# Optimization experiments

Measured on AMD Instinct MI355X. Metric: run time of the kernel, lower is better.

The kernel has to match this reference:

```python
import jax, jax.numpy as jnp
import numpy as np

N = 50000
E = 1600000
F_IN = 128
F_OUT = 64
NEG_SLOPE = 0.2


def setup_inputs() -> dict:
    key = jax.random.key(0)
    k1, k2, k3, k4, k5, k6 = jax.random.split(key, 6)
    x = jax.random.normal(k1, (N, F_IN), dtype=jnp.float32)
    edge_index = jax.random.randint(k2, (2, E), 0, N, dtype=jnp.int64)
    # GATConv params (heads=1): glorot-ish scale
    W = jax.random.normal(k3, (F_IN, F_OUT), dtype=jnp.float32) * (1.0 / np.sqrt(F_IN))
    att_src = jax.random.normal(k4, (F_OUT,), dtype=jnp.float32) * (1.0 / np.sqrt(F_OUT))
    att_dst = jax.random.normal(k5, (F_OUT,), dtype=jnp.float32) * (1.0 / np.sqrt(F_OUT))
    bias = jnp.zeros((F_OUT,), dtype=jnp.float32)
    return {"x": x, "edge_index": edge_index, "W": W, "att_src": att_src, "att_dst": att_dst, "bias": bias}


def _gat_forward(x, edge_index, W, att_src, att_dst, bias):
    n = x.shape[0]
    # add self loops (PyG GATConv default)
    loops = jnp.arange(n, dtype=edge_index.dtype)
    src = jnp.concatenate([edge_index[0], loops])  # [E+N]
    dst = jnp.concatenate([edge_index[1], loops])  # [E+N]

    h = x @ W                                      # [N, F_OUT]
    a_src = h @ att_src                            # [N]
    a_dst = h @ att_dst                            # [N]

    e = a_src[src] + a_dst[dst]                    # [E+N]
    e = jnp.where(e > 0, e, NEG_SLOPE * e)         # LeakyReLU(0.2)

    # softmax over edges grouped by destination node
    e_max = jax.ops.segment_max(e, dst, num_segments=n)     # [N]
    e_exp = jnp.exp(e - e_max[dst])                          # [E+N]
    e_sum = jax.ops.segment_sum(e_exp, dst, num_segments=n)  # [N]
    alpha = e_exp / e_sum[dst]                               # [E+N]

    msg = h[src] * alpha[:, None]                            # [E+N, F_OUT]
    out = jax.ops.segment_sum(msg, dst, num_segments=n)      # [N, F_OUT]
    out = out + bias
    return jax.nn.relu(out)


def reference(x, edge_index, W, att_src, att_dst, bias):
    return _gat_forward(x, edge_index, W, att_src, att_dst, bias)
```

## Files before the change

### kernel.cpp

```cpp
#include <hip/hip_runtime.h>

#define NN 50000
#define NE 1600000
#define FIN 128
#define FOUT 64
#define SLOPE 0.2f

#define NB   1563
#define NPB  32
#define CAPB 1536
#define FBLK 261
#define CHC4 1536
#define GBLK 782
#define LW   136

typedef unsigned int u32;
typedef short short8 __attribute__((ext_vector_type(8)));
typedef float f32x4 __attribute__((ext_vector_type(4)));

__device__ __forceinline__ unsigned short f2bf(float f) {
    u32 u = __float_as_uint(f);
    u += 0x7FFFu + ((u >> 16) & 1u);
    return (unsigned short)(u >> 16);
}
__device__ __forceinline__ float bf2f(unsigned short s) {
    return __uint_as_float(((u32)s) << 16);
}

union FusedLds {
    unsigned short Wt[64 * LW];
    struct { int lc[NB]; int lb[NB]; } f;
};

__global__ __launch_bounds__(256) void fused_k(
        const float* __restrict__ x, const float* __restrict__ W,
        const float* __restrict__ att_s, const float* __restrict__ att_d,
        const int* __restrict__ ei, int* __restrict__ bcur,
        u32* __restrict__ staging, unsigned short* __restrict__ h,
        float* __restrict__ a_src, float* __restrict__ a_dst) {
    __shared__ FusedLds L;
    const int tid = threadIdx.x;

    if (blockIdx.x < FBLK) {
        int* lc = L.f.lc; int* lb = L.f.lb;
        for (int j = tid; j < NB; j += 256) lc[j] = 0;
        __syncthreads();
        const int4* sd4 = (const int4*)(ei + NE);
        const int4* ss4 = (const int4*)ei;
        const int lo = blockIdx.x * CHC4, hi = min(NE / 4, lo + CHC4);
        for (int i = lo + tid; i < hi; i += 256) {
            int4 d = sd4[i];
            atomicAdd(&lc[d.x >> 5], 1);
            atomicAdd(&lc[d.y >> 5], 1);
            atomicAdd(&lc[d.z >> 5], 1);
            atomicAdd(&lc[d.w >> 5], 1);
        }
        __syncthreads();
        for (int j = tid; j < NB; j += 256) {
            int c = lc[j];
            lb[j] = c ? atomicAdd(&bcur[j], c) : 0;
        }
        __syncthreads();
        for (int j = tid; j < NB; j += 256) lc[j] = 0;
        __syncthreads();
        for (int i = lo + tid; i < hi; i += 256) {
            int4 d = sd4[i];
            int4 s = ss4[i];
            int b, pos;
            b = d.x >> 5; pos = lb[b] + atomicAdd(&lc[b], 1);
            if (pos < CAPB) staging[b * CAPB + pos] = (u32)s.x | ((u32)(d.x & 31) << 16);
            b = d.y >> 5; pos = lb[b] + atomicAdd(&lc[b], 1);
            if (pos < CAPB) staging[b * CAPB + pos] = (u32)s.y | ((u32)(d.y & 31) << 16);
            b = d.z >> 5; pos = lb[b] + atomicAdd(&lc[b], 1);
            if (pos < CAPB) staging[b * CAPB + pos] = (u32)s.z | ((u32)(d.z & 31) << 16);
            b = d.w >> 5; pos = lb[b] + atomicAdd(&lc[b], 1);
            if (pos < CAPB) staging[b * CAPB + pos] = (u32)s.w | ((u32)(d.w & 31) << 16);
        }
    } else {
        unsigned short* Wt = L.Wt;
        const int node0 = (blockIdx.x - FBLK) * 64;
        for (int i = tid; i < 128 * 16; i += 256) {
            int k = i >> 4, f = (i & 15) * 4;
            float4 w4 = ((const float4*)W)[i];
            Wt[(f + 0) * LW + k] = f2bf(w4.x);
            Wt[(f + 1) * LW + k] = f2bf(w4.y);
            Wt[(f + 2) * LW + k] = f2bf(w4.z);
            Wt[(f + 3) * LW + k] = f2bf(w4.w);
        }

        const int wv = tid >> 6, lane = tid & 63;
        const int q = lane >> 4, mr = lane & 15;
        const int row = node0 + wv * 16 + mr;
        const bool valid = row < NN;
        const float4* x4 = (const float4*)x;

        short8 afr[4];
        #pragma unroll
        for (int ks = 0; ks < 4; ++ks) {
            float4 f0 = make_float4(0.f, 0.f, 0.f, 0.f), f1 = f0;
            if (valid) {
                f0 = x4[(size_t)row * 32 + ks * 8 + q * 2];
                f1 = x4[(size_t)row * 32 + ks * 8 + q * 2 + 1];
            }
            short8 a;
            a[0] = (short)f2bf(f0.x); a[1] = (short)f2bf(f0.y);
            a[2] = (short)f2bf(f0.z); a[3] = (short)f2bf(f0.w);
            a[4] = (short)f2bf(f1.x); a[5] = (short)f2bf(f1.y);
            a[6] = (short)f2bf(f1.z); a[7] = (short)f2bf(f1.w);
            afr[ks] = a;
        }
        __syncthreads();

        f32x4 acc[4] = {{0,0,0,0},{0,0,0,0},{0,0,0,0},{0,0,0,0}};
        #pragma unroll
        for (int ks = 0; ks < 4; ++ks) {
            #pragma unroll
            for (int nt = 0; nt < 4; ++nt) {
                short8 b = *(const short8*)(Wt + (nt * 16 + mr) * LW + ks * 32 + q * 8);
                acc[nt] = __builtin_amdgcn_mfma_f32_16x16x32_bf16(afr[ks], b, acc[nt], 0, 0, 0);
            }
        }
        float atts[4], attd[4];
        #pragma unroll
        for (int nt = 0; nt < 4; ++nt) {
            atts[nt] = att_s[nt * 16 + mr];
            attd[nt] = att_d[nt * 16 + mr];
        }
        #pragma unroll
        for (int r = 0; r < 4; ++r) {
            int node = node0 + wv * 16 + q * 4 + r;
            float ps = 0.f, pd = 0.f;
            #pragma unroll
            for (int nt = 0; nt < 4; ++nt) {
                float v = acc[nt][r];
                if (node < NN) h[(size_t)node * 64 + nt * 16 + mr] = f2bf(v);
                ps += v * atts[nt];
                pd += v * attd[nt];
            }
            #pragma unroll
            for (int off = 8; off > 0; off >>= 1) {
                ps += __shfl_xor(ps, off);
                pd += __shfl_xor(pd, off);
            }
            if (mr == 0 && node < NN) { a_src[node] = ps; a_dst[node] = pd; }
        }
    }
}

__global__ __launch_bounds__(256) void agg_k(
        const u32* __restrict__ staging, const int* __restrict__ bcur,
        const float* __restrict__ a_src, const float* __restrict__ a_dst,
        const ushort4* __restrict__ h4, const float* __restrict__ bias,
        float* __restrict__ out) {
    const int bkt = blockIdx.x;
    const int node0 = bkt << 5;
    const int nNodes = min(NPB, NN - node0);
    const int bsize = min(bcur[bkt], CAPB);
    const u32* stg = staging + bkt * CAPB;
    const int tid = threadIdx.x, wv = tid >> 6, lane = tid & 63;

    __shared__ u32 pk[CAPB];
    __shared__ unsigned short ssrc[CAPB];
    __shared__ int lcnt[NPB];
    __shared__ int lbase[NPB + 1];
    __shared__ int lcur[NPB];
    float* evals = (float*)pk;

    for (int j = tid; j < bsize; j += 256) pk[j] = stg[j];
    if (tid < NPB) lcnt[tid] = 0;
    __syncthreads();
    for (int j = tid; j < bsize; j += 256)
        atomicAdd(&lcnt[pk[j] >> 16], 1);
    __syncthreads();
    if (tid < 64) {
        int v = (tid < NPB) ? lcnt[tid] : 0;
        #pragma unroll
        for (int off = 1; off < NPB; off <<= 1) {
            int u = __shfl_up(v, off);
            if (tid >= off) v += u;
        }
        if (tid < NPB) lbase[tid + 1] = v;
        if (tid == 0) lbase[0] = 0;
    }
    if (tid >= 64 && tid < 64 + NPB) lcur[tid - 64] = 0;
    __syncthreads();
    for (int j = tid; j < bsize; j += 256) {
        u32 w = pk[j];
        int ld = w >> 16;
        int pos = lbase[ld] + atomicAdd(&lcur[ld], 1);
        ssrc[pos] = (unsigned short)(w & 0xFFFFu);
    }
    __syncthreads();

    const int q = lane >> 4, ql = lane & 15;
    const float4 b4 = ((const float4*)bias)[ql];
    #pragma unroll
    for (int rnd = 0; rnd < 2; ++rnd) {
        const int ln = rnd * 16 + wv * 4 + q;
        if (ln >= nNodes) continue;
        const int n = node0 + ln;
        const int st = lbase[ln], deg = lbase[ln + 1] - st;
        const float ad = a_dst[n];
        float es = a_src[n] + ad; es = es > 0.f ? es : SLOPE * es;
        const float ps = __expf(es);
        float sum = 0.f;
        for (int j = ql; j < deg; j += 16) {
            int s = ssrc[st + j];
            float e = a_src[s] + ad; e = e > 0.f ? e : SLOPE * e;
            float pe = __expf(e);
            evals[st + j] = pe;
            sum += pe;
        }
        sum += __shfl_xor(sum, 8); sum += __shfl_xor(sum, 4);
        sum += __shfl_xor(sum, 2); sum += __shfl_xor(sum, 1);
        const float inv = 1.f / (sum + ps);

        ushort4 hs = h4[(size_t)n * 16 + ql];
        float a0 = ps * bf2f(hs.x), a1 = ps * bf2f(hs.y);
        float a2 = ps * bf2f(hs.z), a3 = ps * bf2f(hs.w);
        int j = 0;
        for (; j + 4 <= deg; j += 4) {
            int s0 = ssrc[st + j], s1 = ssrc[st + j + 1];
            int s2 = ssrc[st + j + 2], s3 = ssrc[st + j + 3];
            float e0 = evals[st + j], e1 = evals[st + j + 1];
            float e2 = evals[st + j + 2], e3 = evals[st + j + 3];
            ushort4 v0 = h4[(size_t)s0 * 16 + ql];
            ushort4 v1 = h4[(size_t)s1 * 16 + ql];
            ushort4 v2 = h4[(size_t)s2 * 16 + ql];
            ushort4 v3 = h4[(size_t)s3 * 16 + ql];
            a0 += e0 * bf2f(v0.x); a1 += e0 * bf2f(v0.y);
            a2 += e0 * bf2f(v0.z); a3 += e0 * bf2f(v0.w);
            a0 += e1 * bf2f(v1.x); a1 += e1 * bf2f(v1.y);
            a2 += e1 * bf2f(v1.z); a3 += e1 * bf2f(v1.w);
            a0 += e2 * bf2f(v2.x); a1 += e2 * bf2f(v2.y);
            a2 += e2 * bf2f(v2.z); a3 += e2 * bf2f(v2.w);
            a0 += e3 * bf2f(v3.x); a1 += e3 * bf2f(v3.y);
            a2 += e3 * bf2f(v3.z); a3 += e3 * bf2f(v3.w);
        }
        for (; j < deg; ++j) {
            int s = ssrc[st + j];
            float ev = evals[st + j];
            ushort4 hv = h4[(size_t)s * 16 + ql];
            a0 += ev * bf2f(hv.x); a1 += ev * bf2f(hv.y);
            a2 += ev * bf2f(hv.z); a3 += ev * bf2f(hv.w);
        }
        float4 o;
        o.x = a0 * inv + b4.x; o.x = o.x > 0.f ? o.x : 0.f;
        o.y = a1 * inv + b4.y; o.y = o.y > 0.f ? o.y : 0.f;
        o.z = a2 * inv + b4.z; o.z = o.z > 0.f ? o.z : 0.f;
        o.w = a3 * inv + b4.w; o.w = o.w > 0.f ? o.w : 0.f;
        ((float4*)out)[(size_t)n * 16 + ql] = o;
    }
}

extern "C" void kernel_launch(void* const* d_in, const int* in_sizes, int n_in,
                              void* d_out, int out_size, void* d_ws, size_t ws_size,
                              hipStream_t stream) {
    const float* x     = (const float*)d_in[0];
    const int*   ei    = (const int*)d_in[1];
    const float* W     = (const float*)d_in[2];
    const float* att_s = (const float*)d_in[3];
    const float* att_d = (const float*)d_in[4];
    const float* bias  = (const float*)d_in[5];
    float* out = (float*)d_out;

    unsigned short* h = (unsigned short*)d_ws;
    float* a_src  = (float*)(h + (size_t)NN * 64);
    float* a_dst  = a_src + NN;
    int*   bcur   = (int*)(a_dst + NN);
    u32*   staging = (u32*)(bcur + 2048);

    hipMemsetAsync(bcur, 0, NB * sizeof(int), stream);

    fused_k<<<FBLK + GBLK, 256, 0, stream>>>(x, W, att_s, att_d, ei, bcur,
                                             staging, h, a_src, a_dst);
    agg_k<<<NB, 256, 0, stream>>>(staging, bcur, a_src, a_dst,
                                  (const ushort4*)h, bias, out);
}
```

Before: 145.6 us.

## Replace single-pass bucket scatter with two-level coarse/fine radix partition of edges

Edge bucketing by destination now runs in two passes. A coarse pass scatters edges into 63 bins of 800 nodes each, with small per-wave LDS histograms, and a new fine_k kernel splits each bin into 32-node buckets for the aggregation kernel. The aim is to cut the global atomic traffic and scattered writes of the old scheme, which kept 1563 per-block counters and did one global atomic per bucket per block. The cost is an extra kernel launch and an extra read/write pass over the staged edges. Bucket capacity limits remain, so overflowing buckets would still silently drop edges.

```diff
diff --git a/kernel.cpp b/kernel.cpp
--- a/kernel.cpp
+++ b/kernel.cpp
@@ -6,12 +6,16 @@
 #define FOUT 64
 #define SLOPE 0.2f
 
-#define NB   1563
+#define NBC  63
+#define NPC  800
+#define CAPC 27500
+#define NBF  1575
 #define NPB  32
 #define CAPB 1536
 #define FBLK 261
 #define CHC4 1536
 #define GBLK 782
+#define K2PB 8
 #define LW   136
 
 typedef unsigned int u32;
@@ -29,52 +33,52 @@
 
 union FusedLds {
     unsigned short Wt[64 * LW];
-    struct { int lc[NB]; int lb[NB]; } f;
+    struct { int cnt[4][64]; int gb[64]; int cur[64]; } f;
 };
 
 __global__ __launch_bounds__(256) void fused_k(
         const float* __restrict__ x, const float* __restrict__ W,
         const float* __restrict__ att_s, const float* __restrict__ att_d,
-        const int* __restrict__ ei, int* __restrict__ bcur,
-        u32* __restrict__ staging, unsigned short* __restrict__ h,
+        const int* __restrict__ ei, int* __restrict__ ccur,
+        u32* __restrict__ cstage, unsigned short* __restrict__ h,
         float* __restrict__ a_src, float* __restrict__ a_dst) {
     __shared__ FusedLds L;
     const int tid = threadIdx.x;
 
     if (blockIdx.x < FBLK) {
-        int* lc = L.f.lc; int* lb = L.f.lb;
-        for (int j = tid; j < NB; j += 256) lc[j] = 0;
+        const int wv = tid >> 6;
+        ((int*)L.f.cnt)[tid] = 0;
         __syncthreads();
         const int4* sd4 = (const int4*)(ei + NE);
         const int4* ss4 = (const int4*)ei;
         const int lo = blockIdx.x * CHC4, hi = min(NE / 4, lo + CHC4);
         for (int i = lo + tid; i < hi; i += 256) {
             int4 d = sd4[i];
-            atomicAdd(&lc[d.x >> 5], 1);
-            atomicAdd(&lc[d.y >> 5], 1);
-            atomicAdd(&lc[d.z >> 5], 1);
-            atomicAdd(&lc[d.w >> 5], 1);
+            atomicAdd(&L.f.cnt[wv][d.x / NPC], 1);
+            atomicAdd(&L.f.cnt[wv][d.y / NPC], 1);
+            atomicAdd(&L.f.cnt[wv][d.z / NPC], 1);
+            atomicAdd(&L.f.cnt[wv][d.w / NPC], 1);
         }
         __syncthreads();
-        for (int j = tid; j < NB; j += 256) {
-            int c = lc[j];
-            lb[j] = c ? atomicAdd(&bcur[j], c) : 0;
-        }
-        __syncthreads();
-        for (int j = tid; j < NB; j += 256) lc[j] = 0;
+        if (tid < NBC) {
+            int tot = L.f.cnt[0][tid] + L.f.cnt[1][tid]
+                    + L.f.cnt[2][tid] + L.f.cnt[3][tid];
+            L.f.gb[tid] = tot ? atomicAdd(&ccur[tid], tot) : 0;
+            L.f.cur[tid] = 0;
+        }
         __syncthreads();
         for (int i = lo + tid; i < hi; i += 256) {
             int4 d = sd4[i];
             int4 s = ss4[i];
             int b, pos;
-            b = d.x >> 5; pos = lb[b] + atomicAdd(&lc[b], 1);
-            if (pos < CAPB) staging[b * CAPB + pos] = (u32)s.x | ((u32)(d.x & 31) << 16);
-            b = d.y >> 5; pos = lb[b] + atomicAdd(&lc[b], 1);
-            if (pos < CAPB) staging[b * CAPB + pos] = (u32)s.y | ((u32)(d.y & 31) << 16);
-            b = d.z >> 5; pos = lb[b] + atomicAdd(&lc[b], 1);
-            if (pos < CAPB) staging[b * CAPB + pos] = (u32)s.z | ((u32)(d.z & 31) << 16);
-            b = d.w >> 5; pos = lb[b] + atomicAdd(&lc[b], 1);
-            if (pos < CAPB) staging[b * CAPB + pos] = (u32)s.w | ((u32)(d.w & 31) << 16);
+            b = d.x / NPC; pos = L.f.gb[b] + atomicAdd(&L.f.cur[b], 1);
+            if (pos < CAPC) cstage[b * CAPC + pos] = (u32)s.x | ((u32)(d.x - b * NPC) << 16);
+            b = d.y / NPC; pos = L.f.gb[b] + atomicAdd(&L.f.cur[b], 1);
+            if (pos < CAPC) cstage[b * CAPC + pos] = (u32)s.y | ((u32)(d.y - b * NPC) << 16);
+            b = d.z / NPC; pos = L.f.gb[b] + atomicAdd(&L.f.cur[b], 1);
+            if (pos < CAPC) cstage[b * CAPC + pos] = (u32)s.z | ((u32)(d.z - b * NPC) << 16);
+            b = d.w / NPC; pos = L.f.gb[b] + atomicAdd(&L.f.cur[b], 1);
+            if (pos < CAPC) cstage[b * CAPC + pos] = (u32)s.w | ((u32)(d.w - b * NPC) << 16);
         }
     } else {
         unsigned short* Wt = L.Wt;
@@ -87,7 +91,6 @@
             Wt[(f + 2) * LW + k] = f2bf(w4.z);
             Wt[(f + 3) * LW + k] = f2bf(w4.w);
         }
-
         const int wv = tid >> 6, lane = tid & 63;
         const int q = lane >> 4, mr = lane & 15;
         const int row = node0 + wv * 16 + mr;
@@ -147,6 +150,41 @@
     }
 }
 
+__global__ __launch_bounds__(256) void fine_k(
+        const u32* __restrict__ cstage, const int* __restrict__ ccur,
+        int* __restrict__ fcur, u32* __restrict__ fstage) {
+    const int bin = blockIdx.x / K2PB, sub = blockIdx.x % K2PB;
+    const int size = min(ccur[bin], CAPC);
+    const int qs = (size + K2PB - 1) / K2PB;
+    const int lo = sub * qs, hi = min(size, lo + qs);
+    const u32* src = cstage + (size_t)bin * CAPC;
+    const int tid = threadIdx.x, wv = tid >> 6;
+
+    __shared__ int cnt[4][32];
+    __shared__ int gb[32];
+    __shared__ int cur[32];
+    ((int*)cnt)[tid & 127] = 0;
+    __syncthreads();
+    for (int i = lo + tid; i < hi; i += 256)
+        atomicAdd(&cnt[wv][(src[i] >> 16) >> 5], 1);
+    __syncthreads();
+    if (tid < 25) {
+        int tot = cnt[0][tid] + cnt[1][tid] + cnt[2][tid] + cnt[3][tid];
+        gb[tid] = tot ? atomicAdd(&fcur[bin * 25 + tid], tot) : 0;
+        cur[tid] = 0;
+    }
+    __syncthreads();
+    for (int i = lo + tid; i < hi; i += 256) {
+        u32 w = src[i];
+        int dl = w >> 16;
+        int f = dl >> 5;
+        int pos = gb[f] + atomicAdd(&cur[f], 1);
+        if (pos < CAPB)
+            fstage[(size_t)(bin * 25 + f) * CAPB + pos] =
+                (w & 0xFFFFu) | ((u32)(dl & 31) << 16);
+    }
+}
+
 __global__ __launch_bounds__(256) void agg_k(
         const u32* __restrict__ staging, const int* __restrict__ bcur,
         const float* __restrict__ a_src, const float* __restrict__ a_dst,
@@ -154,9 +192,10 @@
         float* __restrict__ out) {
     const int bkt = blockIdx.x;
     const int node0 = bkt << 5;
+    if (node0 >= NN) return;
     const int nNodes = min(NPB, NN - node0);
     const int bsize = min(bcur[bkt], CAPB);
-    const u32* stg = staging + bkt * CAPB;
+    const u32* stg = staging + (size_t)bkt * CAPB;
     const int tid = threadIdx.x, wv = tid >> 6, lane = tid & 63;
 
     __shared__ u32 pk[CAPB];
@@ -267,13 +306,16 @@
     unsigned short* h = (unsigned short*)d_ws;
     float* a_src  = (float*)(h + (size_t)NN * 64);
     float* a_dst  = a_src + NN;
-    int*   bcur   = (int*)(a_dst + NN);
-    u32*   staging = (u32*)(bcur + 2048);
-
-    hipMemsetAsync(bcur, 0, NB * sizeof(int), stream);
-
-    fused_k<<<FBLK + GBLK, 256, 0, stream>>>(x, W, att_s, att_d, ei, bcur,
-                                             staging, h, a_src, a_dst);
-    agg_k<<<NB, 256, 0, stream>>>(staging, bcur, a_src, a_dst,
-                                  (const ushort4*)h, bias, out);
-}
+    int*   ccur   = (int*)(a_dst + NN);
+    int*   fcur   = ccur + 64;
+    u32*   cstage = (u32*)(fcur + 1600);
+    u32*   fstage = cstage + (size_t)NBC * CAPC;
+
+    hipMemsetAsync(ccur, 0, (64 + 1600) * sizeof(int), stream);
+
+    fused_k<<<FBLK + GBLK, 256, 0, stream>>>(x, W, att_s, att_d, ei, ccur,
+                                             cstage, h, a_src, a_dst);
+    fine_k<<<NBC * K2PB, 256, 0, stream>>>(cstage, ccur, fcur, fstage);
+    agg_k<<<NBF, 256, 0, stream>>>(fstage, fcur, a_src, a_dst,
+                                   (const ushort4*)h, bias, out);
+}
```

After: 145.2 us. No clear change (-0.3%).
